# Performance work log

Hardware: AMD Instinct MI355X
Metric: run time of the kernel (lower is better)

Reference implementation:

```python
import jax, jax.numpy as jnp
import numpy as np
from jax import lax

B, N, E, CIN, COUT, H, W, KS = 32, 32, 128, 64, 128, 128, 128, 3


def setup_inputs() -> dict:
    key = jax.random.key(0)
    ks = jax.random.split(key, 12)
    xav = lambda k, shape: jax.random.normal(k, shape, jnp.float32) * np.sqrt(2.0 / (shape[0] + shape[1]))
    return {
        "game_board": jax.random.randint(ks[0], (B, H, W), 0, N, jnp.int32),
        "state": jax.random.normal(ks[1], (B, CIN, H, W), jnp.float32),
        "node_embeds": jax.random.normal(ks[2], (N, E), jnp.float32),
        "goal_embed": jax.random.normal(ks[3], (B, E), jnp.float32),
        "char_to_node": jnp.arange(N, dtype=jnp.int32),
        "conv_w": jax.random.normal(ks[4], (COUT, CIN, KS, KS), jnp.float32) * np.sqrt(1.0 / (CIN * KS * KS)),
        "conv_b": jnp.zeros((COUT,), jnp.float32),
        "wQ": xav(ks[5], (2 * E, E)),
        "wK": xav(ks[6], (2 * E, E)),
        "wV": xav(ks[7], (2 * E, E)),
        "final_w": xav(ks[8], (COUT, E)),  # torch Linear weight [out, in]
        "final_b": jnp.zeros((COUT,), jnp.float32),
    }


def reference(game_board, state, node_embeds, goal_embed, char_to_node,
              conv_w, conv_b, wQ, wK, wV, final_w, final_b):
    # Conv2d, stride 1, padding kernel//2 -> same spatial size. [B,COUT,H,W]
    pad = KS // 2
    conv_out = lax.conv_general_dilated(
        state, conv_w, (1, 1), [(pad, pad), (pad, pad)],
        dimension_numbers=("NCHW", "OIHW", "NCHW")) + conv_b[None, :, None, None]

    # Node attention: cat(node, goal) along feature dim -> [B,N,2E]
    node_b = jnp.broadcast_to(node_embeds[None], (B, N, E))
    goal_b = jnp.broadcast_to(goal_embed[:, None, :], (B, N, E))
    x = jnp.concatenate([node_b, goal_b], axis=-1)  # [B,N,2E]
    Q = jnp.einsum("bnf,fk->bnk", x, wQ)
    K = jnp.einsum("bnf,fk->bnk", x, wK)
    V = jnp.einsum("bnf,fk->bnk", x, wV)
    scores = jnp.einsum("bqk,bnk->bqn", Q, K) / np.sqrt(float(E))
    atten = jnp.einsum("bqn,bnk->bqk", jax.nn.softmax(scores, axis=-1), V)  # [B,N,E]
    out_node = jnp.einsum("bnk,ok->bno", atten, final_w) + final_b  # [B,N,COUT]

    # embed_state: place node embedding at every grid cell whose char maps to that node.
    # char_to_node is the inverse of node_2_game_char (identity here); one gather per cell.
    node_idx = char_to_node[game_board]  # [B,H,W]
    gathered = jnp.take_along_axis(
        out_node, node_idx.reshape(B, H * W, 1), axis=1).reshape(B, H, W, COUT)
    valid = ((game_board >= 0) & (game_board < N)).astype(gathered.dtype)[..., None]
    out = conv_out.transpose(0, 2, 3, 1) + gathered * valid  # [B,H,W,COUT]
    return out.transpose(0, 3, 1, 2)  # [B,COUT,H,W]
```

## Files before the change

### kernel.cpp

```cpp
#include <hip/hip_runtime.h>
#include <hip/hip_bf16.h>

#define B_    32
#define N_    32
#define E_    128
#define CIN_  64
#define COUT_ 128
#define H_    128
#define W_    128

using bf16x8 = __attribute__((ext_vector_type(8))) short;
using f32x4  = __attribute__((ext_vector_type(4))) float;

static __device__ __forceinline__ unsigned short f2bf(float f) {
  union { float f; unsigned u; } v; v.f = f;
  unsigned r = v.u + 0x7FFFu + ((v.u >> 16) & 1u);
  return (unsigned short)(r >> 16);
}

static __device__ __forceinline__ void gl2lds16(const void* g, void* l) {
  __builtin_amdgcn_global_load_lds(
      (const __attribute__((address_space(1))) unsigned int*)g,
      (__attribute__((address_space(3))) unsigned int*)l, 16, 0, 0);
}

__global__ __launch_bounds__(256) void prep_kernel(
    const float* __restrict__ state, const float* __restrict__ node_embeds,
    const float* __restrict__ goal_embed, const float* __restrict__ conv_w,
    const float* __restrict__ wQ, const float* __restrict__ wK,
    const float* __restrict__ wV,
    short* __restrict__ nhwc, short* __restrict__ Wp, float* __restrict__ qkv) {
  __shared__ __align__(16) unsigned char smem[33280];
  int bid = blockIdx.x, tid = threadIdx.x;

  if (bid < 4096) {
    int b = bid >> 7, y = bid & 127;
    unsigned* lds = (unsigned*)smem;
    int cp = tid >> 3;
    int xo = (tid & 7) << 4;
    const float* r0 = state + (((b * 64 + 2 * cp) * 128 + y) * 128) + xo;
    const float* r1 = r0 + 16384;
    float4 a0[4], a1[4];
#pragma unroll
    for (int j = 0; j < 4; ++j) { a0[j] = *(const float4*)(r0 + 4 * j); a1[j] = *(const float4*)(r1 + 4 * j); }
    int k16 = cp >> 2;
    const float* f0 = (const float*)a0;
    const float* f1 = (const float*)a1;
#pragma unroll
    for (int jj = 0; jj < 16; ++jj) {
      int x = xo + jj;
      unsigned pk = (unsigned)f2bf(f0[jj]) | ((unsigned)f2bf(f1[jj]) << 16);
      lds[x * 32 + (((k16 + x + 1) & 7) << 2) + (cp & 3)] = pk;
    }
    __syncthreads();
    int cell = tid >> 1, h = tid & 1;
    unsigned* rowbase = (unsigned*)nhwc + (size_t)((b * 130 + y + 1) * 136) * 32;
    unsigned* dst = rowbase + (cell + 1) * 32 + h * 16;
    unsigned* src = lds + cell * 32 + h * 16;
#pragma unroll
    for (int k = 0; k < 4; ++k) *(uint4*)(dst + 4 * k) = *(uint4*)(src + 4 * k);
    if (tid < 32) rowbase[tid] = 0;
    else rowbase[129 * 32 + (tid - 32)] = 0;
  } else if (bid < 4160) {
    int idx = bid - 4096;
    int b = idx >> 1, yp = (idx & 1) ? 129 : 0;
    unsigned* rowbase = (unsigned*)nhwc + (size_t)((b * 130 + yp) * 136) * 32;
    for (int k = tid; k < 136 * 32; k += 256) rowbase[k] = 0;
  } else if (bid < 4448) {
    int idx = (bid - 4160) * 256 + tid;
    if (idx < COUT_ * CIN_ * 9) {
      int cout = idx / (CIN_ * 9);
      int rem  = idx % (CIN_ * 9);
      int ci   = rem / 9;
      int tap  = rem % 9;
      Wp[(tap * COUT_ + cout) * CIN_ + ci] = (short)f2bf(conv_w[idx]);
    }
  } else {
    int idx = bid - 4448;
    int kg = idx & 7;
    int r  = idx >> 3;
    int b  = r / 3;
    int mat = r - b * 3;
    const float* W = (mat == 0) ? wQ : (mat == 1) ? wK : wV;
    float (*x)[260] = (float(*)[260])smem;
    for (int e = tid; e < 4096; e += 256) x[e >> 7][e & 127] = node_embeds[e];
    for (int e = tid; e < 4096; e += 256) x[e >> 7][128 + (e & 127)] = goal_embed[b * 128 + (e & 127)];
    __syncthreads();
    int k  = kg * 16 + (tid & 15);
    int n0 = tid >> 4, n1 = n0 + 16;
    float a0 = 0.f, a1 = 0.f;
    for (int f = 0; f < 256; f += 4) {
      float4 xv0 = *(const float4*)&x[n0][f];
      float4 xv1 = *(const float4*)&x[n1][f];
      float w0 = W[(f + 0) * 128 + k];
      float w1 = W[(f + 1) * 128 + k];
      float w2 = W[(f + 2) * 128 + k];
      float w3 = W[(f + 3) * 128 + k];
      a0 += xv0.x * w0 + xv0.y * w1 + xv0.z * w2 + xv0.w * w3;
      a1 += xv1.x * w0 + xv1.y * w1 + xv1.z * w2 + xv1.w * w3;
    }
    int base = (mat * 32 + b) * 32;
    qkv[(base + n0) * 128 + k] = a0;
    qkv[(base + n1) * 128 + k] = a1;
  }
}

__global__ void attn_kernel(const float* __restrict__ qkv, float* __restrict__ atten) {
  __shared__ float QS[32][132], KS[32][132], VS[32][132];
  __shared__ float S[32][33];
  int tid = threadIdx.x, b = blockIdx.x;
  const float* q0 = qkv + b * 4096;
  const float* k0 = qkv + 131072 + b * 4096;
  const float* v0 = qkv + 262144 + b * 4096;
  for (int e = tid; e < 4096; e += 256) {
    int n = e >> 7, k = e & 127;
    QS[n][k] = q0[e]; KS[n][k] = k0[e]; VS[n][k] = v0[e];
  }
  __syncthreads();
  for (int p = tid; p < 1024; p += 256) {
    int qi = p >> 5, ni = p & 31;
    float acc = 0.f;
    for (int k = 0; k < 128; k += 4) {
      float4 a = *(const float4*)&QS[qi][k];
      float4 c = *(const float4*)&KS[ni][k];
      acc += a.x * c.x + a.y * c.y + a.z * c.z + a.w * c.w;
    }
    S[qi][ni] = acc * 0.08838834764831845f;
  }
  __syncthreads();
  if (tid < 32) {
    float mx = -1e30f;
    for (int n = 0; n < 32; ++n) mx = fmaxf(mx, S[tid][n]);
    float sum = 0.f;
    for (int n = 0; n < 32; ++n) { float e = __expf(S[tid][n] - mx); S[tid][n] = e; sum += e; }
    float inv = 1.f / sum;
    for (int n = 0; n < 32; ++n) S[tid][n] *= inv;
  }
  __syncthreads();
  int qi = tid >> 3, ks = (tid & 7) * 16;
  float4 A0 = {0,0,0,0}, A1 = {0,0,0,0}, A2 = {0,0,0,0}, A3 = {0,0,0,0};
  for (int n = 0; n < 32; ++n) {
    float p = S[qi][n];
    float4 v_0 = *(const float4*)&VS[n][ks];
    float4 v_1 = *(const float4*)&VS[n][ks + 4];
    float4 v_2 = *(const float4*)&VS[n][ks + 8];
    float4 v_3 = *(const float4*)&VS[n][ks + 12];
    A0.x += p * v_0.x; A0.y += p * v_0.y; A0.z += p * v_0.z; A0.w += p * v_0.w;
    A1.x += p * v_1.x; A1.y += p * v_1.y; A1.z += p * v_1.z; A1.w += p * v_1.w;
    A2.x += p * v_2.x; A2.y += p * v_2.y; A2.z += p * v_2.z; A2.w += p * v_2.w;
    A3.x += p * v_3.x; A3.y += p * v_3.y; A3.z += p * v_3.z; A3.w += p * v_3.w;
  }
  float* op = atten + (b * 32 + qi) * 128 + ks;
  *(float4*)&op[0] = A0; *(float4*)&op[4] = A1; *(float4*)&op[8] = A2; *(float4*)&op[12] = A3;
}

__global__ void final_kernel(const float* __restrict__ atten, const float* __restrict__ fw,
                             const float* __restrict__ fb, float* __restrict__ out_node) {
  __shared__ float ar[128];
  int tid = threadIdx.x;
  int n = blockIdx.x, b = blockIdx.y;
  ar[tid] = atten[(b * 32 + n) * 128 + tid];
  __syncthreads();
  const float* fr = fw + tid * 128;
  float acc = fb[tid];
  for (int k = 0; k < 128; k += 4) {
    float4 f = *(const float4*)&fr[k];
    acc += ar[k] * f.x + ar[k + 1] * f.y + ar[k + 2] * f.z + ar[k + 3] * f.w;
  }
  out_node[(b * 32 + n) * 128 + tid] = acc;
}

#define XC 72
__global__ __launch_bounds__(256) void conv_kernel(
    const short* __restrict__ nhwc, const float* __restrict__ conv_b,
    const int* __restrict__ game_board, const int* __restrict__ char_to_node,
    const short* __restrict__ Wp, const float* __restrict__ out_node,
    float* __restrict__ out) {
  __shared__ __align__(16) short tile[4 * XC * 64];
  int tid = threadIdx.x;
  int lane = tid & 63, wave = tid >> 6;
  int y0 = blockIdx.x * 2;
  int x0 = blockIdx.y * 64;
  int b  = blockIdx.z;

  {
    const short* grow = nhwc + (size_t)((b * 130 + y0 + wave) * 136 + x0) * 64;
    short* lrow = tile + wave * (XC * 64);
#pragma unroll
    for (int ch = 0; ch < 9; ++ch)
      gl2lds16(grow + ch * 512 + lane * 8, lrow + ch * 512 + lane * 8);
  }

  int q = lane >> 4, i = lane & 15;
  int mtset = (wave >> 1) * 4;
  int ty    = wave & 1;
  int gy    = y0 + ty;

  int nidx[4]; bool gval[4];
#pragma unroll
  for (int ntl = 0; ntl < 4; ++ntl) {
    int gx = x0 + ntl * 16 + i;
    int gb = game_board[(b * 128 + gy) * 128 + gx];
    gval[ntl] = (gb >= 0 && gb < 32);
    int nn = gval[ntl] ? char_to_node[gb] : 0;
    nidx[ntl] = nn < 0 ? 0 : (nn > 31 ? 31 : nn);
  }

  f32x4 acc[4][4];
#pragma unroll
  for (int m = 0; m < 4; ++m)
#pragma unroll
    for (int n = 0; n < 4; ++n) acc[m][n] = (f32x4){0.f, 0.f, 0.f, 0.f};

  const short* wbase = Wp + i * 64 + q * 8;
  bf16x8 aR[3][4];
#pragma unroll
  for (int m = 0; m < 4; ++m) aR[0][m] = *(const bf16x8*)(wbase + (mtset + m) * 1024);
#pragma unroll
  for (int m = 0; m < 4; ++m) aR[1][m] = *(const bf16x8*)(wbase + 32 + (mtset + m) * 1024);

  __syncthreads();

#pragma unroll
  for (int chunk = 0; chunk < 18; ++chunk) {
    int t = chunk >> 1, h = chunk & 1;
    int kh = t / 3, kw = t - kh * 3;
    int row = ty + kh;
    bf16x8 bF[4];
#pragma unroll
    for (int ntl = 0; ntl < 4; ++ntl) {
      int c = ntl * 16 + i + kw;
      bF[ntl] = *(const bf16x8*)(tile + (row * XC + c) * 64 + (((h * 4 + q + c) & 7) << 3));
    }
    if (chunk < 16) {
      int c2 = chunk + 2;
      const short* wb2 = wbase + (c2 >> 1) * 8192 + (c2 & 1) * 32;
#pragma unroll
      for (int m = 0; m < 4; ++m) aR[(chunk + 2) % 3][m] = *(const bf16x8*)(wb2 + (mtset + m) * 1024);
    }
#pragma unroll
    for (int m = 0; m < 4; ++m)
#pragma unroll
      for (int n = 0; n < 4; ++n)
        acc[m][n] = __builtin_amdgcn_mfma_f32_16x16x32_bf16(aR[chunk % 3][m], bF[n], acc[m][n], 0, 0, 0);
  }

  float* tbuf = (float*)tile;
#pragma unroll
  for (int p = 0; p < 2; ++p) {
    __syncthreads();
    if ((wave >> 1) == p) {
#pragma unroll
      for (int ntl = 0; ntl < 4; ++ntl) {
        const float* gn = out_node + (b * 32 + nidx[ntl]) * 128;
        bool valid = gval[ntl];
#pragma unroll
        for (int m = 0; m < 4; ++m) {
          int c0 = (mtset + m) * 16 + q * 4;
          float4 bias = *(const float4*)(conv_b + c0);
          float4 g = valid ? *(const float4*)(gn + c0) : make_float4(0.f, 0.f, 0.f, 0.f);
          f32x4 a = acc[m][ntl];
          int base = (m * 16 + q * 4) * 132 + ty * 64 + ntl * 16 + i;
          tbuf[base]       = a[0] + bias.x + g.x;
          tbuf[base + 132] = a[1] + bias.y + g.y;
          tbuf[base + 264] = a[2] + bias.z + g.z;
          tbuf[base + 396] = a[3] + bias.w + g.w;
        }
      }
    }
    __syncthreads();
#pragma unroll
    for (int it = 0; it < 8; ++it) {
      int f  = tid + it * 256;
      int cp_ = f >> 5, rem = f & 31;
      int row = rem >> 4, xq = rem & 15;
      float4 v = *(const float4*)&tbuf[cp_ * 132 + row * 64 + xq * 4];
      int c = p * 64 + cp_;
      int addr = (b * 128 + c) * 16384 + (y0 + row) * 128 + x0 + xq * 4;
      *(float4*)&out[addr] = v;
    }
  }
}

extern "C" void kernel_launch(void* const* d_in, const int* in_sizes, int n_in,
                              void* d_out, int out_size, void* d_ws, size_t ws_size,
                              hipStream_t stream) {
  const int*   game_board   = (const int*)  d_in[0];
  const float* state        = (const float*)d_in[1];
  const float* node_embeds  = (const float*)d_in[2];
  const float* goal_embed   = (const float*)d_in[3];
  const int*   char_to_node = (const int*)  d_in[4];
  const float* conv_w       = (const float*)d_in[5];
  const float* conv_b       = (const float*)d_in[6];
  const float* wQ           = (const float*)d_in[7];
  const float* wK           = (const float*)d_in[8];
  const float* wV           = (const float*)d_in[9];
  const float* final_w      = (const float*)d_in[10];
  const float* final_b      = (const float*)d_in[11];
  float* out = (float*)d_out;

  char* ws = (char*)d_ws;
  short* Wp       = (short*)(ws);
  float* qkv      = (float*)(ws + 147456);
  float* atten    = (float*)(ws + 1720320);
  float* out_node = (float*)(ws + 2244608);
  short* nhwc     = (short*)(ws + 2768896);

  hipLaunchKernelGGL(prep_kernel, dim3(5216), dim3(256), 0, stream,
                     state, node_embeds, goal_embed, conv_w, wQ, wK, wV, nhwc, Wp, qkv);
  hipLaunchKernelGGL(attn_kernel, dim3(32), dim3(256), 0, stream, qkv, atten);
  hipLaunchKernelGGL(final_kernel, dim3(32, 32), dim3(128), 0, stream, atten, final_w, final_b, out_node);
  hipLaunchKernelGGL(conv_kernel, dim3(64, 2, 32), dim3(256), 0, stream,
                     nhwc, conv_b, game_board, char_to_node, Wp, out_node, out);
}
```

Baseline: 616.8 us.

## Fuse NCHW-to-bf16 NHWC conversion into conv tile load, drop padded intermediate

The separate prep pass that converted state to a padded bf16 NHWC buffer is removed. The conv kernel now reads fp32 NCHW state directly, converts it with packed bf16 conversion and writes it into its swizzled LDS tile, handling halo and zero padding in place. This removes a full write and re-read of the intermediate activation buffer. In exchange, each block re-reads overlapping halo rows from fp32 and gives up the asynchronous global-to-LDS loads. The QKV projection also splits the goal half of the input, computing its dot product once per output column instead of once per node.

```diff
diff --git a/kernel.cpp b/kernel.cpp
--- a/kernel.cpp
+++ b/kernel.cpp
@@ -18,56 +18,17 @@
   return (unsigned short)(r >> 16);
 }
 
-static __device__ __forceinline__ void gl2lds16(const void* g, void* l) {
-  __builtin_amdgcn_global_load_lds(
-      (const __attribute__((address_space(1))) unsigned int*)g,
-      (__attribute__((address_space(3))) unsigned int*)l, 16, 0, 0);
-}
-
 __global__ __launch_bounds__(256) void prep_kernel(
-    const float* __restrict__ state, const float* __restrict__ node_embeds,
-    const float* __restrict__ goal_embed, const float* __restrict__ conv_w,
+    const float* __restrict__ node_embeds, const float* __restrict__ goal_embed,
+    const float* __restrict__ conv_w,
     const float* __restrict__ wQ, const float* __restrict__ wK,
     const float* __restrict__ wV,
-    short* __restrict__ nhwc, short* __restrict__ Wp, float* __restrict__ qkv) {
-  __shared__ __align__(16) unsigned char smem[33280];
+    short* __restrict__ Wp, float* __restrict__ qkv) {
+  __shared__ __align__(16) float xs[32][132];
   int bid = blockIdx.x, tid = threadIdx.x;
 
-  if (bid < 4096) {
-    int b = bid >> 7, y = bid & 127;
-    unsigned* lds = (unsigned*)smem;
-    int cp = tid >> 3;
-    int xo = (tid & 7) << 4;
-    const float* r0 = state + (((b * 64 + 2 * cp) * 128 + y) * 128) + xo;
-    const float* r1 = r0 + 16384;
-    float4 a0[4], a1[4];
-#pragma unroll
-    for (int j = 0; j < 4; ++j) { a0[j] = *(const float4*)(r0 + 4 * j); a1[j] = *(const float4*)(r1 + 4 * j); }
-    int k16 = cp >> 2;
-    const float* f0 = (const float*)a0;
-    const float* f1 = (const float*)a1;
-#pragma unroll
-    for (int jj = 0; jj < 16; ++jj) {
-      int x = xo + jj;
-      unsigned pk = (unsigned)f2bf(f0[jj]) | ((unsigned)f2bf(f1[jj]) << 16);
-      lds[x * 32 + (((k16 + x + 1) & 7) << 2) + (cp & 3)] = pk;
-    }
-    __syncthreads();
-    int cell = tid >> 1, h = tid & 1;
-    unsigned* rowbase = (unsigned*)nhwc + (size_t)((b * 130 + y + 1) * 136) * 32;
-    unsigned* dst = rowbase + (cell + 1) * 32 + h * 16;
-    unsigned* src = lds + cell * 32 + h * 16;
-#pragma unroll
-    for (int k = 0; k < 4; ++k) *(uint4*)(dst + 4 * k) = *(uint4*)(src + 4 * k);
-    if (tid < 32) rowbase[tid] = 0;
-    else rowbase[129 * 32 + (tid - 32)] = 0;
-  } else if (bid < 4160) {
-    int idx = bid - 4096;
-    int b = idx >> 1, yp = (idx & 1) ? 129 : 0;
-    unsigned* rowbase = (unsigned*)nhwc + (size_t)((b * 130 + yp) * 136) * 32;
-    for (int k = tid; k < 136 * 32; k += 256) rowbase[k] = 0;
-  } else if (bid < 4448) {
-    int idx = (bid - 4160) * 256 + tid;
+  if (bid < 288) {
+    int idx = bid * 256 + tid;
     if (idx < COUT_ * CIN_ * 9) {
       int cout = idx / (CIN_ * 9);
       int rem  = idx % (CIN_ * 9);
@@ -76,29 +37,35 @@
       Wp[(tap * COUT_ + cout) * CIN_ + ci] = (short)f2bf(conv_w[idx]);
     }
   } else {
-    int idx = bid - 4448;
+    int idx = bid - 288;
     int kg = idx & 7;
     int r  = idx >> 3;
     int b  = r / 3;
     int mat = r - b * 3;
     const float* W = (mat == 0) ? wQ : (mat == 1) ? wK : wV;
-    float (*x)[260] = (float(*)[260])smem;
-    for (int e = tid; e < 4096; e += 256) x[e >> 7][e & 127] = node_embeds[e];
-    for (int e = tid; e < 4096; e += 256) x[e >> 7][128 + (e & 127)] = goal_embed[b * 128 + (e & 127)];
+    for (int e = tid; e < 4096; e += 256) xs[e >> 7][e & 127] = node_embeds[e];
     __syncthreads();
     int k  = kg * 16 + (tid & 15);
     int n0 = tid >> 4, n1 = n0 + 16;
-    float a0 = 0.f, a1 = 0.f;
-    for (int f = 0; f < 256; f += 4) {
-      float4 xv0 = *(const float4*)&x[n0][f];
-      float4 xv1 = *(const float4*)&x[n1][f];
+    const float* gb_ = goal_embed + b * 128;
+    float a0 = 0.f, a1 = 0.f, s2 = 0.f;
+    for (int f = 0; f < 128; f += 4) {
+      float4 xv0 = *(const float4*)&xs[n0][f];
+      float4 xv1 = *(const float4*)&xs[n1][f];
       float w0 = W[(f + 0) * 128 + k];
       float w1 = W[(f + 1) * 128 + k];
       float w2 = W[(f + 2) * 128 + k];
       float w3 = W[(f + 3) * 128 + k];
       a0 += xv0.x * w0 + xv0.y * w1 + xv0.z * w2 + xv0.w * w3;
       a1 += xv1.x * w0 + xv1.y * w1 + xv1.z * w2 + xv1.w * w3;
-    }
+      float4 gv = *(const float4*)&gb_[f];
+      float u0 = W[(128 + f) * 128 + k];
+      float u1 = W[(129 + f) * 128 + k];
+      float u2 = W[(130 + f) * 128 + k];
+      float u3 = W[(131 + f) * 128 + k];
+      s2 += gv.x * u0 + gv.y * u1 + gv.z * u2 + gv.w * u3;
+    }
+    a0 += s2; a1 += s2;
     int base = (mat * 32 + b) * 32;
     qkv[(base + n0) * 128 + k] = a0;
     qkv[(base + n1) * 128 + k] = a1;
@@ -172,7 +139,7 @@
 
 #define XC 72
 __global__ __launch_bounds__(256) void conv_kernel(
-    const short* __restrict__ nhwc, const float* __restrict__ conv_b,
+    const float* __restrict__ state, const float* __restrict__ conv_b,
     const int* __restrict__ game_board, const int* __restrict__ char_to_node,
     const short* __restrict__ Wp, const float* __restrict__ out_node,
     float* __restrict__ out) {
@@ -183,12 +150,51 @@
   int x0 = blockIdx.y * 64;
   int b  = blockIdx.z;
 
+  unsigned* lds32 = (unsigned*)tile;
+
   {
-    const short* grow = nhwc + (size_t)((b * 130 + y0 + wave) * 136 + x0) * 64;
-    short* lrow = tile + wave * (XC * 64);
-#pragma unroll
-    for (int ch = 0; ch < 9; ++ch)
-      gl2lds16(grow + ch * 512 + lane * 8, lrow + ch * 512 + lane * 8);
+    int cp  = tid >> 3;
+    int xo  = (tid & 7) << 3;
+    int k16 = cp >> 2;
+    const float* sbase = state + (size_t)(b * 64 + 2 * cp) * 16384;
+#pragma unroll
+    for (int r = 0; r < 4; ++r) {
+      int y = y0 + r - 1;
+      bool yv = (unsigned)y < 128u;
+      float e0[8], e1[8];
+      if (yv) {
+        const float* p0 = sbase + y * 128 + x0 + xo;
+        const float* p1 = p0 + 16384;
+        *(float4*)&e0[0] = *(const float4*)p0;
+        *(float4*)&e0[4] = *(const float4*)(p0 + 4);
+        *(float4*)&e1[0] = *(const float4*)p1;
+        *(float4*)&e1[4] = *(const float4*)(p1 + 4);
+      } else {
+#pragma unroll
+        for (int j = 0; j < 8; ++j) { e0[j] = 0.f; e1[j] = 0.f; }
+      }
+#pragma unroll
+      for (int j = 0; j < 8; ++j) {
+        int c = xo + j + 1;
+        unsigned pk;
+        asm("v_cvt_pk_bf16_f32 %0, %1, %2" : "=v"(pk) : "v"(e0[j]), "v"(e1[j]));
+        lds32[((r * XC + c) << 5) + (((k16 + c) & 7) << 2) + (cp & 3)] = pk;
+      }
+    }
+    int side = tid >> 7;
+    int rem  = tid & 127;
+    int r2   = rem >> 5, cq = rem & 31;
+    int c    = side ? 65 : 0;
+    int x    = x0 + (side ? 64 : -1);
+    int y    = y0 + r2 - 1;
+    float h0 = 0.f, h1 = 0.f;
+    if ((unsigned)x < 128u && (unsigned)y < 128u) {
+      const float* p = state + (size_t)(b * 64 + 2 * cq) * 16384 + y * 128 + x;
+      h0 = p[0]; h1 = p[16384];
+    }
+    unsigned pk;
+    asm("v_cvt_pk_bf16_f32 %0, %1, %2" : "=v"(pk) : "v"(h0), "v"(h1));
+    lds32[((r2 * XC + c) << 5) + ((((cq >> 2) + c) & 7) << 2) + (cq & 3)] = pk;
   }
 
   int q = lane >> 4, i = lane & 15;
@@ -304,12 +310,11 @@
   float* qkv      = (float*)(ws + 147456);
   float* atten    = (float*)(ws + 1720320);
   float* out_node = (float*)(ws + 2244608);
-  short* nhwc     = (short*)(ws + 2768896);
-
-  hipLaunchKernelGGL(prep_kernel, dim3(5216), dim3(256), 0, stream,
-                     state, node_embeds, goal_embed, conv_w, wQ, wK, wV, nhwc, Wp, qkv);
+
+  hipLaunchKernelGGL(prep_kernel, dim3(1056), dim3(256), 0, stream,
+                     node_embeds, goal_embed, conv_w, wQ, wK, wV, Wp, qkv);
   hipLaunchKernelGGL(attn_kernel, dim3(32), dim3(256), 0, stream, qkv, atten);
   hipLaunchKernelGGL(final_kernel, dim3(32, 32), dim3(128), 0, stream, atten, final_w, final_b, out_node);
   hipLaunchKernelGGL(conv_kernel, dim3(64, 2, 32), dim3(256), 0, stream,
-                     nhwc, conv_b, game_board, char_to_node, Wp, out_node, out);
-}
+                     state, conv_b, game_board, char_to_node, Wp, out_node, out);
+}
```

Result: faster. 592.1 us (-4.0%).
